# Optimization experiments

Measured on AMD Instinct MI355X. Metric: run time of the kernel, lower is better.

## Reference

```python
import jax, jax.numpy as jnp
import numpy as np

TWO_PI = 2.0 * np.pi
LN_EPS = 1e-5


def _periods(out_dim, nb):
    # periods[i,j,g] = i*(out_dim*nb) + j*nb + g + 2
    return jnp.arange(out_dim * out_dim * nb, dtype=jnp.float32).reshape(out_dim, out_dim, nb) + 2.0


def _layer(x, M, gamma, beta, P, residual):
    # x: (B,S,in), M: (out,in), P: (out,out,nb)
    out_dim, _, nb = P.shape
    S = x.shape[1]
    xt = jnp.matmul(x, M.T)  # (B,S,out)
    mu = jnp.mean(xt, axis=-1, keepdims=True)
    var = jnp.mean((xt - mu) ** 2, axis=-1, keepdims=True)
    xn = (xt - mu) / jnp.sqrt(var + LN_EPS) * gamma + beta
    pos = jnp.arange(S, dtype=jnp.float32)[:, None, None, None]  # (S,1,1,1)
    phi = jnp.cos(TWO_PI * pos / _periods(out_dim, nb)[None])  # (S,out,out,nb)
    W = jnp.einsum('ijg,sijg->sij', P, phi)  # (S,out,out) contract basis first
    Nk = jnp.einsum('bsj,sij->bsi', xn, W)  # (B,S,out)
    return Nk + residual


def setup_inputs() -> dict:
    key = jax.random.key(0)
    ks = jax.random.split(key, 8)
    B, S, D_in, D, NB = 8, 1024, 64, 96, 8
    u = lambda k, shape, a: jax.random.uniform(k, shape, jnp.float32, -a, a)
    return {
        'seq': jax.random.normal(ks[0], (B, S, D_in), jnp.float32),
        'M1': u(ks[1], (D, D_in), 0.5),
        'P1': u(ks[2], (D, D, NB), 0.1),
        'Wres1': u(ks[3], (D, D_in), 0.1),
        'g1': jnp.ones((D,), jnp.float32),
        'b1': jnp.zeros((D,), jnp.float32),
        'M2': u(ks[4], (D, D), 0.5),
        'P2': u(ks[5], (D, D, NB), 0.1),
        'g2': jnp.ones((D,), jnp.float32),
        'b2': jnp.zeros((D,), jnp.float32),
    }


def reference(seq, M1, P1, Wres1, g1, b1, M2, P2, g2, b2):
    # Layer 1: 64 -> 96, 'separate' residual uses a Linear projection
    x1 = _layer(seq, M1, g1, b1, P1, jnp.matmul(seq, Wres1.T))
    # Layer 2: 96 -> 96, 'separate' residual with in_dim==out_dim is Identity
    x2 = _layer(x1, M2, g2, b2, P2, x1)
    return x2
```

## Files before the change

kernel.cpp:

```cpp
#include <hip/hip_runtime.h>
#include <hip/hip_fp16.h>

#define S_LEN    1024
#define B_SZ     8
#define D_IN     64
#define D_OUT    96
#define NB       8
#define NE       (D_OUT * D_OUT)
#define CHUNK    32
#define NCHUNK   (S_LEN / CHUNK)
#define NT_W     256
#define NWBLK    (NCHUNK * (NE / NT_W))
#define NT_C     512
#define HPAD     104
#define SPAD     100
#define XPAD     68

__device__ __forceinline__ float cos_rev(float v) {
    v -= floorf(v);
    return __builtin_amdgcn_cosf(v);
}

__global__ void __launch_bounds__(NT_W)
w_kernel(const float* __restrict__ P1, const float* __restrict__ P2,
         __half* __restrict__ W1, __half* __restrict__ W2) {
    const int c  = blockIdx.x / (NE / NT_W);
    const int eb = blockIdx.x % (NE / NT_W);
    const int e  = eb * NT_W + threadIdx.x;
    const int s0 = c * CHUNK;
    const float s0f = (float)s0;

    float p1l[NB], p2l[NB];
    *(float4*)&p1l[0] = *(const float4*)(P1 + e * NB);
    *(float4*)&p1l[4] = *(const float4*)(P1 + e * NB + 4);
    *(float4*)&p2l[0] = *(const float4*)(P2 + e * NB);
    *(float4*)&p2l[4] = *(const float4*)(P2 + e * NB + 4);

    float cc[NB], cp[NB], kk[NB];
    #pragma unroll
    for (int g = 0; g < NB; ++g) {
        const float inv = __builtin_amdgcn_rcpf((float)(e * NB + 2 + g));
        cc[g] = cos_rev(s0f * inv);
        cp[g] = cos_rev((s0f - 1.0f) * inv);
        kk[g] = 2.0f * __builtin_amdgcn_cosf(inv);
    }

    #pragma unroll 4
    for (int s = s0; s < s0 + CHUNK; ++s) {
        float a1 = 0.0f, a2 = 0.0f;
        #pragma unroll
        for (int g = 0; g < NB; ++g) {
            a1 = fmaf(p1l[g], cc[g], a1);
            a2 = fmaf(p2l[g], cc[g], a2);
        }
        W1[s * NE + e] = __float2half(a1);
        W2[s * NE + e] = __float2half(a2);
        #pragma unroll
        for (int g = 0; g < NB; ++g) {
            float cn = fmaf(kk[g], cc[g], -cp[g]);
            cp[g] = cc[g];
            cc[g] = cn;
        }
    }
}

__device__ __forceinline__ float nkdot(const __half* __restrict__ wrow,
                                       const float* __restrict__ xr) {
    float acc = 0.0f;
    #pragma unroll
    for (int h = 0; h < 2; ++h) {
        #pragma unroll
        for (int j = h * 6; j < h * 6 + 6; ++j) {
            float4 raw = *(const float4*)(wrow + 8 * j);
            const __half2* hp = (const __half2*)&raw;
            float2 c0 = __half22float2(hp[0]);
            float2 c1 = __half22float2(hp[1]);
            float2 c2 = __half22float2(hp[2]);
            float2 c3 = __half22float2(hp[3]);
            float4 x0 = *(const float4*)(xr + 8 * j);
            float4 x1 = *(const float4*)(xr + 8 * j + 4);
            acc = fmaf(c0.x, x0.x, acc); acc = fmaf(c0.y, x0.y, acc);
            acc = fmaf(c1.x, x0.z, acc); acc = fmaf(c1.y, x0.w, acc);
            acc = fmaf(c2.x, x1.x, acc); acc = fmaf(c2.y, x1.y, acc);
            acc = fmaf(c3.x, x1.z, acc); acc = fmaf(c3.y, x1.w, acc);
        }
    }
    return acc;
}

__device__ __forceinline__ void stage_W(__half* __restrict__ wh,
                                        const __half* __restrict__ Wg,
                                        int tid) {
    for (int cidx = tid; cidx < NE / 8; cidx += NT_C) {
        const int i = cidx / 12;
        const int j = (cidx % 12) * 8;
        *(float4*)(wh + i * HPAD + j) = *(const float4*)(Wg + cidx * 8);
    }
}

__global__ void __launch_bounds__(NT_C)
consumer(const float* __restrict__ seq,
         const float* __restrict__ M1, const float* __restrict__ Wres1,
         const float* __restrict__ M2,
         const float* __restrict__ g1, const float* __restrict__ b1,
         const float* __restrict__ g2, const float* __restrict__ b2,
         const __half* __restrict__ W1g, const __half* __restrict__ W2g,
         float* __restrict__ out) {
    __shared__ __align__(16) __half wh [D_OUT * HPAD];
    __shared__ __align__(16) float  xn [B_SZ * SPAD];
    __shared__ __align__(16) float  x1b[B_SZ * SPAD];

    const int s   = blockIdx.x;
    const int tid = threadIdx.x;

    {
        int b = tid >> 6, k = tid & 63;
        x1b[b * SPAD + k] = seq[((size_t)b * S_LEN + s) * D_IN + k];
    }
    __syncthreads();

    stage_W(wh, W1g + (size_t)s * NE, tid);

    float ar0 = 0.0f, ar1 = 0.0f;
    for (int pass = 0; pass < 2; ++pass) {
        int idx = tid + pass * NT_C;
        if (idx >= B_SZ * D_OUT) break;
        int i = idx >> 3, b = idx & 7;
        const float4* m  = (const float4*)(M1 + i * D_IN);
        const float4* wr = (const float4*)(Wres1 + i * D_IN);
        const float*  xr = x1b + b * SPAD;
        float at = 0.0f, ar = 0.0f;
        #pragma unroll
        for (int k = 0; k < D_IN / 4; ++k) {
            float4 mv = m[k], rv = wr[k];
            float x0 = xr[4*k], x1 = xr[4*k+1], x2 = xr[4*k+2], x3 = xr[4*k+3];
            at = fmaf(mv.x, x0, fmaf(mv.y, x1, fmaf(mv.z, x2, fmaf(mv.w, x3, at))));
            ar = fmaf(rv.x, x0, fmaf(rv.y, x1, fmaf(rv.z, x2, fmaf(rv.w, x3, ar))));
        }
        xn[b * SPAD + i] = at;
        if (pass == 0) ar0 = ar; else ar1 = ar;
    }
    __syncthreads();

    {
        const int b = tid >> 6, lane = tid & 63;
        const bool lo = (lane < 32);
        float* row = xn + b * SPAD;
        float v0 = row[lane];
        float v1 = lo ? row[64 + lane] : 0.0f;
        float sum = v0 + v1, sq = fmaf(v0, v0, v1 * v1);
        #pragma unroll
        for (int off = 32; off > 0; off >>= 1) {
            sum += __shfl_down(sum, off, 64);
            sq  += __shfl_down(sq,  off, 64);
        }
        sum = __shfl(sum, 0, 64);
        sq  = __shfl(sq,  0, 64);
        const float mu  = sum * (1.0f / 96.0f);
        const float var = fmaf(sq, 1.0f / 96.0f, -(mu * mu));
        const float rs  = rsqrtf(var + 1e-5f);
        row[lane] = fmaf((v0 - mu) * rs, g1[lane], b1[lane]);
        if (lo) row[64 + lane] = fmaf((v1 - mu) * rs, g1[64 + lane], b1[64 + lane]);
    }
    __syncthreads();

    for (int pass = 0; pass < 2; ++pass) {
        int idx = tid + pass * NT_C;
        if (idx >= B_SZ * D_OUT) break;
        int i = idx >> 3, b = idx & 7;
        float ar = (pass == 0) ? ar0 : ar1;
        x1b[b * SPAD + i] = ar + nkdot(wh + i * HPAD, xn + b * SPAD);
    }
    __syncthreads();

    stage_W(wh, W2g + (size_t)s * NE, tid);

    for (int pass = 0; pass < 2; ++pass) {
        int idx = tid + pass * NT_C;
        if (idx >= B_SZ * D_OUT) break;
        int i = idx >> 3, b = idx & 7;
        const float4* m  = (const float4*)(M2 + i * D_OUT);
        const float*  xr = x1b + b * SPAD;
        float at = 0.0f;
        #pragma unroll
        for (int k = 0; k < D_OUT / 4; ++k) {
            float4 mv = m[k];
            at = fmaf(mv.x, xr[4*k], fmaf(mv.y, xr[4*k+1],
                 fmaf(mv.z, xr[4*k+2], fmaf(mv.w, xr[4*k+3], at))));
        }
        xn[b * SPAD + i] = at;
    }
    __syncthreads();

    {
        const int b = tid >> 6, lane = tid & 63;
        const bool lo = (lane < 32);
        float* row = xn + b * SPAD;
        float v0 = row[lane];
        float v1 = lo ? row[64 + lane] : 0.0f;
        float sum = v0 + v1, sq = fmaf(v0, v0, v1 * v1);
        #pragma unroll
        for (int off = 32; off > 0; off >>= 1) {
            sum += __shfl_down(sum, off, 64);
            sq  += __shfl_down(sq,  off, 64);
        }
        sum = __shfl(sum, 0, 64);
        sq  = __shfl(sq,  0, 64);
        const float mu  = sum * (1.0f / 96.0f);
        const float var = fmaf(sq, 1.0f / 96.0f, -(mu * mu));
        const float rs  = rsqrtf(var + 1e-5f);
        row[lane] = fmaf((v0 - mu) * rs, g2[lane], b2[lane]);
        if (lo) row[64 + lane] = fmaf((v1 - mu) * rs, g2[64 + lane], b2[64 + lane]);
    }
    __syncthreads();

    for (int pass = 0; pass < 2; ++pass) {
        int idx = tid + pass * NT_C;
        if (idx >= B_SZ * D_OUT) break;
        int i = idx >> 3, b = idx & 7;
        float acc = nkdot(wh + i * HPAD, xn + b * SPAD);
        out[((size_t)b * S_LEN + s) * D_OUT + i] = acc + x1b[b * SPAD + i];
    }
}

__global__ void __launch_bounds__(NT_W)
hier_fallback(const float* __restrict__ seq,  const float* __restrict__ M1,
              const float* __restrict__ P1,   const float* __restrict__ Wres1,
              const float* __restrict__ g1,   const float* __restrict__ b1,
              const float* __restrict__ M2,   const float* __restrict__ P2,
              const float* __restrict__ g2,   const float* __restrict__ b2,
              float* __restrict__ out) {
    __shared__ __align__(16) float w[D_OUT * SPAD];
    __shared__ __align__(16) float xin[B_SZ * XPAD];
    __shared__ __align__(16) float xn [B_SZ * SPAD];
    __shared__ __align__(16) float x1b[B_SZ * SPAD];
    const int s = blockIdx.x, tid = threadIdx.x;
    const float sf = (float)s;

    for (int idx = tid; idx < B_SZ * D_IN; idx += NT_W) {
        int b = idx >> 6, k = idx & (D_IN - 1);
        xin[b * XPAD + k] = seq[(b * S_LEN + s) * D_IN + k];
    }
    for (int e = tid; e < NE; e += NT_W) {
        float pl[8];
        *(float4*)&pl[0] = *(const float4*)(P1 + e * NB);
        *(float4*)&pl[4] = *(const float4*)(P1 + e * NB + 4);
        float acc = 0.0f;
        #pragma unroll
        for (int g = 0; g < NB; ++g) {
            float v = sf * __builtin_amdgcn_rcpf((float)(e * NB + 2 + g));
            acc = fmaf(pl[g], cos_rev(v), acc);
        }
        int i = e / D_OUT;
        w[e + (SPAD - D_OUT) * i] = acc;
    }
    __syncthreads();
    for (int idx = tid; idx < B_SZ * D_OUT; idx += NT_W) {
        int i = idx >> 3, b = idx & 7;
        const float4* m  = (const float4*)(M1 + i * D_IN);
        const float4* wr = (const float4*)(Wres1 + i * D_IN);
        const float*  xr = xin + b * XPAD;
        float at = 0.0f, ar = 0.0f;
        #pragma unroll
        for (int k = 0; k < D_IN / 4; ++k) {
            float4 mv = m[k], rv = wr[k];
            float x0 = xr[4*k], x1 = xr[4*k+1], x2 = xr[4*k+2], x3 = xr[4*k+3];
            at = fmaf(mv.x, x0, fmaf(mv.y, x1, fmaf(mv.z, x2, fmaf(mv.w, x3, at))));
            ar = fmaf(rv.x, x0, fmaf(rv.y, x1, fmaf(rv.z, x2, fmaf(rv.w, x3, ar))));
        }
        xn [b * SPAD + i] = at;
        x1b[b * SPAD + i] = ar;
    }
    __syncthreads();
    {
        const int b = tid >> 5, rr = tid & 31;
        float* row = xn + b * SPAD;
        float v0 = row[rr], v1 = row[rr + 32], v2 = row[rr + 64];
        float sum = v0 + v1 + v2, sq = fmaf(v0, v0, fmaf(v1, v1, v2 * v2));
        #pragma unroll
        for (int off = 16; off > 0; off >>= 1) {
            sum += __shfl_down(sum, off, 32);
            sq  += __shfl_down(sq,  off, 32);
        }
        sum = __shfl(sum, 0, 32); sq = __shfl(sq, 0, 32);
        float mu = sum * (1.0f/96.0f), var = fmaf(sq, 1.0f/96.0f, -(mu*mu));
        float rs = rsqrtf(var + 1e-5f);
        row[rr]      = fmaf((v0 - mu) * rs, g1[rr],      b1[rr]);
        row[rr + 32] = fmaf((v1 - mu) * rs, g1[rr + 32], b1[rr + 32]);
        row[rr + 64] = fmaf((v2 - mu) * rs, g1[rr + 64], b1[rr + 64]);
    }
    __syncthreads();
    for (int idx = tid; idx < B_SZ * D_OUT; idx += NT_W) {
        int i = idx >> 3, b = idx & 7;
        const float* wrow = w + i * SPAD;
        const float* xr   = xn + b * SPAD;
        float acc = 0.0f;
        #pragma unroll
        for (int j = 0; j < D_OUT / 4; ++j) {
            float4 wv = *(const float4*)(wrow + 4 * j);
            float4 xv = *(const float4*)(xr + 4 * j);
            acc = fmaf(wv.x, xv.x, fmaf(wv.y, xv.y, fmaf(wv.z, xv.z, fmaf(wv.w, xv.w, acc))));
        }
        x1b[b * SPAD + i] += acc;
    }
    __syncthreads();
    for (int e = tid; e < NE; e += NT_W) {
        float pl[8];
        *(float4*)&pl[0] = *(const float4*)(P2 + e * NB);
        *(float4*)&pl[4] = *(const float4*)(P2 + e * NB + 4);
        float acc = 0.0f;
        #pragma unroll
        for (int g = 0; g < NB; ++g) {
            float v = sf * __builtin_amdgcn_rcpf((float)(e * NB + 2 + g));
            acc = fmaf(pl[g], cos_rev(v), acc);
        }
        int i = e / D_OUT;
        w[e + (SPAD - D_OUT) * i] = acc;
    }
    for (int idx = tid; idx < B_SZ * D_OUT; idx += NT_W) {
        int i = idx >> 3, b = idx & 7;
        const float4* m  = (const float4*)(M2 + i * D_OUT);
        const float*  xr = x1b + b * SPAD;
        float at = 0.0f;
        #pragma unroll
        for (int k = 0; k < D_OUT / 4; ++k) {
            float4 mv = m[k];
            at = fmaf(mv.x, xr[4*k], fmaf(mv.y, xr[4*k+1],
                 fmaf(mv.z, xr[4*k+2], fmaf(mv.w, xr[4*k+3], at))));
        }
        xn[b * SPAD + i] = at;
    }
    __syncthreads();
    {
        const int b = tid >> 5, rr = tid & 31;
        float* row = xn + b * SPAD;
        float v0 = row[rr], v1 = row[rr + 32], v2 = row[rr + 64];
        float sum = v0 + v1 + v2, sq = fmaf(v0, v0, fmaf(v1, v1, v2 * v2));
        #pragma unroll
        for (int off = 16; off > 0; off >>= 1) {
            sum += __shfl_down(sum, off, 32);
            sq  += __shfl_down(sq,  off, 32);
        }
        sum = __shfl(sum, 0, 32); sq = __shfl(sq, 0, 32);
        float mu = sum * (1.0f/96.0f), var = fmaf(sq, 1.0f/96.0f, -(mu*mu));
        float rs = rsqrtf(var + 1e-5f);
        row[rr]      = fmaf((v0 - mu) * rs, g2[rr],      b2[rr]);
        row[rr + 32] = fmaf((v1 - mu) * rs, g2[rr + 32], b2[rr + 32]);
        row[rr + 64] = fmaf((v2 - mu) * rs, g2[rr + 64], b2[rr + 64]);
    }
    __syncthreads();
    for (int idx = tid; idx < B_SZ * D_OUT; idx += NT_W) {
        int i = idx >> 3, b = idx & 7;
        const float* wrow = w + i * SPAD;
        const float* xr   = xn + b * SPAD;
        float acc = 0.0f;
        #pragma unroll
        for (int j = 0; j < D_OUT / 4; ++j) {
            float4 wv = *(const float4*)(wrow + 4 * j);
            float4 xv = *(const float4*)(xr + 4 * j);
            acc = fmaf(wv.x, xv.x, fmaf(wv.y, xv.y, fmaf(wv.z, xv.z, fmaf(wv.w, xv.w, acc))));
        }
        out[(b * S_LEN + s) * D_OUT + i] = acc + x1b[b * SPAD + i];
    }
}

extern "C" void kernel_launch(void* const* d_in, const int* in_sizes, int n_in,
                              void* d_out, int out_size, void* d_ws, size_t ws_size,
                              hipStream_t stream) {
    const float* seq   = (const float*)d_in[0];
    const float* M1    = (const float*)d_in[1];
    const float* P1    = (const float*)d_in[2];
    const float* Wres1 = (const float*)d_in[3];
    const float* g1    = (const float*)d_in[4];
    const float* b1    = (const float*)d_in[5];
    const float* M2    = (const float*)d_in[6];
    const float* P2    = (const float*)d_in[7];
    const float* g2    = (const float*)d_in[8];
    const float* b2    = (const float*)d_in[9];
    float* out = (float*)d_out;

    const size_t need = (size_t)2 * S_LEN * NE * sizeof(__half);
    if (ws_size >= need) {
        __half* W1 = (__half*)d_ws;
        __half* W2 = W1 + (size_t)S_LEN * NE;
        w_kernel<<<dim3(NWBLK), dim3(NT_W), 0, stream>>>(P1, P2, W1, W2);
        consumer<<<dim3(S_LEN), dim3(NT_C), 0, stream>>>(
            seq, M1, Wres1, M2, g1, b1, g2, b2, W1, W2, out);
    } else {
        hier_fallback<<<dim3(S_LEN), dim3(NT_W), 0, stream>>>(
            seq, M1, P1, Wres1, g1, b1, M2, P2, g2, b2, out);
    }
}
```

Baseline: 118.7 us.

## Fuse W generation and consumer into one persistent-ticket kernel with per-chunk flags

Merges the W-generation kernel and the consumer kernel into a single launch. Each block takes a ticket from a global atomic counter: the first tickets produce W chunks and signal a per-chunk flag, and later tickets consume sequence positions after spinning on their chunk's flag. This is meant to overlap W production with consumption and remove the kernel boundary. In exchange it adds a memset launch, atomic spin-waits and fences, and generator blocks now run at 512 threads.

```diff
diff --git a/kernel.cpp b/kernel.cpp
--- a/kernel.cpp
+++ b/kernel.cpp
@@ -9,59 +9,18 @@
 #define NE       (D_OUT * D_OUT)
 #define CHUNK    32
 #define NCHUNK   (S_LEN / CHUNK)
+#define NT_C     512
+#define WPB      (NE / NT_C)
+#define NWBLK_F  (NCHUNK * WPB)
 #define NT_W     256
-#define NWBLK    (NCHUNK * (NE / NT_W))
-#define NT_C     512
 #define HPAD     104
 #define SPAD     100
 #define XPAD     68
+#define FLAG_STRIDE 16
 
 __device__ __forceinline__ float cos_rev(float v) {
     v -= floorf(v);
     return __builtin_amdgcn_cosf(v);
-}
-
-__global__ void __launch_bounds__(NT_W)
-w_kernel(const float* __restrict__ P1, const float* __restrict__ P2,
-         __half* __restrict__ W1, __half* __restrict__ W2) {
-    const int c  = blockIdx.x / (NE / NT_W);
-    const int eb = blockIdx.x % (NE / NT_W);
-    const int e  = eb * NT_W + threadIdx.x;
-    const int s0 = c * CHUNK;
-    const float s0f = (float)s0;
-
-    float p1l[NB], p2l[NB];
-    *(float4*)&p1l[0] = *(const float4*)(P1 + e * NB);
-    *(float4*)&p1l[4] = *(const float4*)(P1 + e * NB + 4);
-    *(float4*)&p2l[0] = *(const float4*)(P2 + e * NB);
-    *(float4*)&p2l[4] = *(const float4*)(P2 + e * NB + 4);
-
-    float cc[NB], cp[NB], kk[NB];
-    #pragma unroll
-    for (int g = 0; g < NB; ++g) {
-        const float inv = __builtin_amdgcn_rcpf((float)(e * NB + 2 + g));
-        cc[g] = cos_rev(s0f * inv);
-        cp[g] = cos_rev((s0f - 1.0f) * inv);
-        kk[g] = 2.0f * __builtin_amdgcn_cosf(inv);
-    }
-
-    #pragma unroll 4
-    for (int s = s0; s < s0 + CHUNK; ++s) {
-        float a1 = 0.0f, a2 = 0.0f;
-        #pragma unroll
-        for (int g = 0; g < NB; ++g) {
-            a1 = fmaf(p1l[g], cc[g], a1);
-            a2 = fmaf(p2l[g], cc[g], a2);
-        }
-        W1[s * NE + e] = __float2half(a1);
-        W2[s * NE + e] = __float2half(a2);
-        #pragma unroll
-        for (int g = 0; g < NB; ++g) {
-            float cn = fmaf(kk[g], cc[g], -cp[g]);
-            cp[g] = cc[g];
-            cc[g] = cn;
-        }
-    }
 }
 
 __device__ __forceinline__ float nkdot(const __half* __restrict__ wrow,
@@ -99,23 +58,81 @@
 }
 
 __global__ void __launch_bounds__(NT_C)
-consumer(const float* __restrict__ seq,
-         const float* __restrict__ M1, const float* __restrict__ Wres1,
-         const float* __restrict__ M2,
-         const float* __restrict__ g1, const float* __restrict__ b1,
-         const float* __restrict__ g2, const float* __restrict__ b2,
-         const __half* __restrict__ W1g, const __half* __restrict__ W2g,
-         float* __restrict__ out) {
+fused(const float* __restrict__ seq,
+      const float* __restrict__ M1, const float* __restrict__ Wres1,
+      const float* __restrict__ M2,
+      const float* __restrict__ g1, const float* __restrict__ b1,
+      const float* __restrict__ g2, const float* __restrict__ b2,
+      const float* __restrict__ P1, const float* __restrict__ P2,
+      __half* __restrict__ W1g, __half* __restrict__ W2g,
+      int* __restrict__ flags,
+      float* __restrict__ out) {
     __shared__ __align__(16) __half wh [D_OUT * HPAD];
     __shared__ __align__(16) float  xn [B_SZ * SPAD];
     __shared__ __align__(16) float  x1b[B_SZ * SPAD];
-
-    const int s   = blockIdx.x;
+    __shared__ int s_ticket;
+
     const int tid = threadIdx.x;
+    if (tid == 0) s_ticket = atomicAdd(flags + 32 * FLAG_STRIDE, 1);
+    __syncthreads();
+    const int t = s_ticket;
+
+    if (t < NWBLK_F) {
+        const int c  = t / WPB;
+        const int eb = t % WPB;
+        const int e  = eb * NT_C + tid;
+        const int s0 = c * CHUNK;
+        const float s0f = (float)s0;
+
+        float p1l[NB], p2l[NB];
+        *(float4*)&p1l[0] = *(const float4*)(P1 + e * NB);
+        *(float4*)&p1l[4] = *(const float4*)(P1 + e * NB + 4);
+        *(float4*)&p2l[0] = *(const float4*)(P2 + e * NB);
+        *(float4*)&p2l[4] = *(const float4*)(P2 + e * NB + 4);
+
+        float cc[NB], cp[NB], kk[NB];
+        #pragma unroll
+        for (int g = 0; g < NB; ++g) {
+            const float inv = __builtin_amdgcn_rcpf((float)(e * NB + 2 + g));
+            cc[g] = cos_rev(s0f * inv);
+            cp[g] = cos_rev((s0f - 1.0f) * inv);
+            kk[g] = 2.0f * __builtin_amdgcn_cosf(inv);
+        }
+
+        #pragma unroll 4
+        for (int s = s0; s < s0 + CHUNK; ++s) {
+            float a1 = 0.0f, a2 = 0.0f;
+            #pragma unroll
+            for (int g = 0; g < NB; ++g) {
+                a1 = fmaf(p1l[g], cc[g], a1);
+                a2 = fmaf(p2l[g], cc[g], a2);
+            }
+            W1g[s * NE + e] = __float2half(a1);
+            W2g[s * NE + e] = __float2half(a2);
+            #pragma unroll
+            for (int g = 0; g < NB; ++g) {
+                float cn = fmaf(kk[g], cc[g], -cp[g]);
+                cp[g] = cc[g];
+                cc[g] = cn;
+            }
+        }
+        __threadfence();
+        __syncthreads();
+        if (tid == 0) atomicAdd(flags + c * FLAG_STRIDE, 1);
+        return;
+    }
+
+    const int s = t - NWBLK_F;
+    const int c = s >> 5;
 
     {
         int b = tid >> 6, k = tid & 63;
         x1b[b * SPAD + k] = seq[((size_t)b * S_LEN + s) * D_IN + k];
+    }
+    if (tid == 0) {
+        while (atomicAdd(flags + c * FLAG_STRIDE, 0) < WPB)
+            __builtin_amdgcn_s_sleep(8);
+        __threadfence();
     }
     __syncthreads();
 
@@ -379,13 +396,16 @@
     const float* b2    = (const float*)d_in[9];
     float* out = (float*)d_out;
 
-    const size_t need = (size_t)2 * S_LEN * NE * sizeof(__half);
+    const size_t wbytes   = (size_t)2 * S_LEN * NE * sizeof(__half);
+    const size_t flagsz   = (size_t)(32 * FLAG_STRIDE + FLAG_STRIDE) * sizeof(int);
+    const size_t need     = wbytes + 4096;
     if (ws_size >= need) {
-        __half* W1 = (__half*)d_ws;
-        __half* W2 = W1 + (size_t)S_LEN * NE;
-        w_kernel<<<dim3(NWBLK), dim3(NT_W), 0, stream>>>(P1, P2, W1, W2);
-        consumer<<<dim3(S_LEN), dim3(NT_C), 0, stream>>>(
-            seq, M1, Wres1, M2, g1, b1, g2, b2, W1, W2, out);
+        __half* W1   = (__half*)d_ws;
+        __half* W2   = W1 + (size_t)S_LEN * NE;
+        int*   flags = (int*)((char*)d_ws + wbytes);
+        hipMemsetAsync(flags, 0, flagsz, stream);
+        fused<<<dim3(NWBLK_F + S_LEN), dim3(NT_C), 0, stream>>>(
+            seq, M1, Wres1, M2, g1, b1, g2, b2, P1, P2, W1, W2, flags, out);
     } else {
         hier_fallback<<<dim3(S_LEN), dim3(NT_W), 0, stream>>>(
             seq, M1, P1, Wres1, g1, b1, M2, P2, g2, b2, out);
```

Result: slower. 299.3 us (+152.3%).
